# Kernel tuning notes

Measured on AMD Instinct MI355X. Metric: run time of the kernel, lower is better.

## Reference

```python
import jax, jax.numpy as jnp
import numpy as np
import math

B, S, HID, NH = 4, 2048, 1024, 16
HD = HID // NH  # head dim = 64


def setup_inputs() -> dict:
    key = jax.random.key(0)
    ks = jax.random.split(key, 8)
    sc = 0.02
    return {
        "x": jax.random.normal(ks[0], (B, S, HID), dtype=jnp.float32),
        "att_mask": jnp.zeros((B, 1, 1, S), dtype=jnp.float32),
        "Wq": jax.random.normal(ks[1], (HID, HID), dtype=jnp.float32) * sc,
        "bq": jax.random.normal(ks[2], (HID,), dtype=jnp.float32) * sc,
        "Wk": jax.random.normal(ks[3], (HID, HID), dtype=jnp.float32) * sc,
        "bk": jax.random.normal(ks[4], (HID,), dtype=jnp.float32) * sc,
        "Wv": jax.random.normal(ks[5], (HID, HID), dtype=jnp.float32) * sc,
        "bv": jax.random.normal(ks[6], (HID,), dtype=jnp.float32) * sc,
    }


def reference(x, att_mask, Wq, bq, Wk, bk, Wv, bv):
    # quant_mode=False path: QuantLinear acts as a plain affine projection
    # (the running min/max stats only calibrate `scale`, which is unused in
    # the float path), and IntSoftmax reduces to a standard softmax.
    q = x @ Wq.T + bq  # [B,S,HID]
    k = x @ Wk.T + bk
    v = x @ Wv.T + bv
    # split heads: [B,S,HID] -> [B,NH,S,HD]
    q = q.reshape(B, S, NH, HD).transpose(0, 2, 1, 3)
    k = k.reshape(B, S, NH, HD).transpose(0, 2, 1, 3)
    v = v.reshape(B, S, NH, HD).transpose(0, 2, 1, 3)
    scores = jnp.einsum("bhqd,bhkd->bhqk", q, k) / math.sqrt(HD) + att_mask
    probs = jax.nn.softmax(scores, axis=-1)  # [B,NH,S,S]
    ctx = jnp.einsum("bhqk,bhkd->bhqd", probs, v)  # [B,NH,S,HD]
    return ctx.transpose(0, 2, 1, 3).reshape(B, S, HID)
```

## Files before the change

### kernel.cpp

```cpp
#include <hip/hip_runtime.h>
#include <hip/hip_bf16.h>
#include <cstdint>
#include <cstddef>

#define BB   4
#define SS   2048
#define HIDD 1024
#define NHH  16
#define HDD  64
#define MM   (BB*SS)
#define L2E  1.4426950408889634f
#define SH4  5.770780163555854f

typedef __bf16    bf16x8 __attribute__((ext_vector_type(8)));
typedef float     f32x4  __attribute__((ext_vector_type(4)));
typedef _Float16  half4  __attribute__((ext_vector_type(4)));
typedef _Float16  half2v __attribute__((ext_vector_type(2)));

__device__ __forceinline__ unsigned short f2b(float f) {
    unsigned u = __builtin_bit_cast(unsigned, f);
    return (unsigned short)((u + 0x7FFFu + ((u >> 16) & 1u)) >> 16);
}

__device__ __forceinline__ half2v pkrtz(float a, float b) {
    return __builtin_bit_cast(half2v, __builtin_amdgcn_cvt_pkrtz(a, b));
}

__device__ __forceinline__ void gl_lds16(const void* g, void* l) {
    __builtin_amdgcn_global_load_lds(
        (const __attribute__((address_space(1))) void*)g,
        (__attribute__((address_space(3))) void*)l, 16, 0, 0);
}

#define NX4 (MM * HIDD / 4)
#define NW4 (HIDD * HIDD / 4)
__global__ __launch_bounds__(256) void cvt_all(
    const float* __restrict__ x,  const float* __restrict__ wq,
    const float* __restrict__ wk, const float* __restrict__ wv,
    unsigned short* __restrict__ xb, unsigned short* __restrict__ wb)
{
    int i = blockIdx.x * 256 + threadIdx.x;
    const float* src; unsigned short* dst; int off;
    if (i < NX4) { src = x; dst = xb; off = i; }
    else {
        int j = i - NX4;
        int w = j >> 18;
        off = j & (NW4 - 1);
        src = (w == 0) ? wq : (w == 1) ? wk : wv;
        dst = wb + (size_t)w * HIDD * HIDD;
    }
    float4 v = reinterpret_cast<const float4*>(src)[off];
    ushort4 o;
    o.x = f2b(v.x); o.y = f2b(v.y); o.z = f2b(v.z); o.w = f2b(v.w);
    reinterpret_cast<ushort4*>(dst)[off] = o;
}

__global__ __launch_bounds__(256, 3) void qkv_gemm(
    const unsigned short* __restrict__ xb,
    const unsigned short* __restrict__ wb,
    const float* __restrict__ bq, const float* __restrict__ bk, const float* __restrict__ bv,
    unsigned short* __restrict__ Qb, unsigned short* __restrict__ Kb,
    _Float16* __restrict__ Vtb)
{
    __shared__ unsigned short lA[128 * 64];
    __shared__ unsigned short lB[128 * 64];

    const int tid  = threadIdx.x;
    const int wave = tid >> 6, lane = tid & 63;
    const int lh   = lane & 15, quad = lane >> 4;
    const int l7   = lh & 7;
    const int m0   = blockIdx.x * 128;
    const int opn  = blockIdx.y;
    const int op   = opn >> 3;
    const int n0   = (opn & 7) * 128;
    const unsigned short* W = wb + (size_t)op * HIDD * HIDD;
    const float* bias = (op == 0) ? bq : (op == 1) ? bk : bv;

    f32x4 acc[4][4];
#pragma unroll
    for (int i = 0; i < 4; i++)
#pragma unroll
        for (int j = 0; j < 4; j++) acc[i][j] = f32x4{0.f, 0.f, 0.f, 0.f};

    const int wm = wave & 1, wn = wave >> 1;
    const unsigned short* srcA = (op == 2) ? lA : lB;
    const unsigned short* srcB = (op == 2) ? lB : lA;
    const int offA = (op == 2) ? wm : wn;
    const int offB = (op == 2) ? wn : wm;

    const int srow = tid >> 3;
    const int sg   = tid & 7;

    for (int k0 = 0; k0 < HIDD; k0 += 64) {
#pragma unroll
        for (int rr = 0; rr < 4; rr++) {
            const int row = srow + rr * 32;
            const int gcol = k0 + ((sg ^ (row & 7)) << 3);
            gl_lds16(&xb[(size_t)(m0 + row) * HIDD + gcol], &lA[row * 64 + sg * 8]);
            gl_lds16(&W [(size_t)(n0 + row) * HIDD + gcol], &lB[row * 64 + sg * 8]);
        }
        __syncthreads();

#pragma unroll
        for (int kk = 0; kk < 2; kk++) {
            bf16x8 aF[4], bF[4];
#pragma unroll
            for (int i = 0; i < 4; i++) {
                const int row = offA * 64 + i * 16 + lh;
                aF[i] = *reinterpret_cast<const bf16x8*>(
                    &srcA[row * 64 + (((kk * 4 + quad) ^ l7) << 3)]);
            }
#pragma unroll
            for (int j = 0; j < 4; j++) {
                const int row = offB * 64 + j * 16 + lh;
                bF[j] = *reinterpret_cast<const bf16x8*>(
                    &srcB[row * 64 + (((kk * 4 + quad) ^ l7) << 3)]);
            }
#pragma unroll
            for (int i = 0; i < 4; i++)
#pragma unroll
                for (int j = 0; j < 4; j++)
                    acc[i][j] = __builtin_amdgcn_mfma_f32_16x16x32_bf16(aF[i], bF[j], acc[i][j], 0, 0, 0);
        }
        __syncthreads();
    }

    if (op == 2) {
#pragma unroll
        for (int j = 0; j < 4; j++) {
            const int n = n0 + offB * 64 + j * 16 + lh;
            const float bvv = bias[n];
            const int h = n >> 6, d = n & 63;
#pragma unroll
            for (int i = 0; i < 4; i++) {
                const int mrow = m0 + offA * 64 + i * 16 + quad * 4;
                const int b_ = mrow >> 11, s_ = mrow & 2047;
                half2v h01 = pkrtz(acc[i][j][0] + bvv, acc[i][j][1] + bvv);
                half2v h23 = pkrtz(acc[i][j][2] + bvv, acc[i][j][3] + bvv);
                half4 hv; hv[0] = h01[0]; hv[1] = h01[1]; hv[2] = h23[0]; hv[3] = h23[1];
                size_t a = ((size_t)(b_ * NHH + h) * HDD + d) * SS + s_;
                *reinterpret_cast<half4*>(&Vtb[a]) = hv;
            }
        }
    } else {
        const float qs = (op == 0) ? (0.125f * L2E) : 1.0f;
        unsigned short* dst = (op == 0) ? Qb : Kb;
#pragma unroll
        for (int i = 0; i < 4; i++) {
            const int nb = n0 + offA * 64 + i * 16 + quad * 4;
            const float4 bb = *reinterpret_cast<const float4*>(&bias[nb]);
            const int h = nb >> 6, d = nb & 63;
#pragma unroll
            for (int j = 0; j < 4; j++) {
                const int m = m0 + offB * 64 + j * 16 + lh;
                const int b_ = m >> 11, s_ = m & 2047;
                ushort4 o;
                o.x = f2b((acc[i][j][0] + bb.x) * qs);
                o.y = f2b((acc[i][j][1] + bb.y) * qs);
                o.z = f2b((acc[i][j][2] + bb.z) * qs);
                o.w = f2b((acc[i][j][3] + bb.w) * qs);
                *reinterpret_cast<ushort4*>(
                    &dst[((size_t)(b_ * NHH + h) * SS + s_) * HDD + d]) = o;
            }
        }
    }
}

__global__ __launch_bounds__(256, 4) void attn_kernel(
    const unsigned short* __restrict__ Qb,
    const unsigned short* __restrict__ Kb,
    const _Float16* __restrict__ Vtb,
    const float* __restrict__ mask,
    float* __restrict__ out)
{
    __shared__ unsigned short lK[2][64 * 64];
    __shared__ _Float16      lV[2][64 * 64];

    const int tid  = threadIdx.x;
    const int wave = tid >> 6, lane = tid & 63;
    const int lh   = lane & 15, quad = lane >> 4;
    const int l7   = lh & 7;
    const int bh = blockIdx.x, qt = blockIdx.y;
    const int b = bh >> 4, h = bh & 15;
    const unsigned short* Qh = Qb  + (size_t)bh * SS * HDD;
    const unsigned short* Kh = Kb  + (size_t)bh * SS * HDD;
    const _Float16*       Vh = Vtb + (size_t)bh * HDD * SS;
    const float* mk = mask + (size_t)b * SS;
    const int q0 = qt * 128;

    bf16x8 qF[2][2];
#pragma unroll
    for (int i = 0; i < 2; i++)
#pragma unroll
        for (int kk = 0; kk < 2; kk++)
            qF[i][kk] = *reinterpret_cast<const bf16x8*>(
                &Qh[(size_t)(q0 + wave * 32 + i * 16 + lh) * HDD + kk * 32 + quad * 8]);

    f32x4 oacc[2][4];
#pragma unroll
    for (int i = 0; i < 2; i++)
#pragma unroll
        for (int dj = 0; dj < 4; dj++) oacc[i][dj] = f32x4{0.f, 0.f, 0.f, 0.f};
    float ls[2] = {0.f, 0.f};

    const int srow = tid >> 3;
    const int sg   = tid & 7;

#define STAGE(KT, BUF) do {                                                     \
    const int kb_ = (KT) * 64;                                                  \
    _Pragma("unroll")                                                           \
    for (int rr = 0; rr < 2; rr++) {                                            \
        const int row = srow + rr * 32;                                         \
        const int sw = ((sg ^ (row & 7)) << 3);                                 \
        gl_lds16(&Kh[(size_t)(kb_ + row) * HDD + sw], &lK[BUF][row * 64 + sg * 8]); \
        gl_lds16(&Vh[(size_t)row * SS + kb_ + sw],    &lV[BUF][row * 64 + sg * 8]); \
    }                                                                           \
} while (0)

    STAGE(0, 0);
    __syncthreads();

    for (int kt = 0; kt < SS / 64; kt++) {
        if (kt < SS / 64 - 1) STAGE(kt + 1, (kt + 1) & 1);
        const int buf = kt & 1;
        const int kb = kt * 64;

        float4 mg[4];
#pragma unroll
        for (int c = 0; c < 4; c++)
            mg[c] = *reinterpret_cast<const float4*>(&mk[kb + c * 16 + quad * 4]);

        half4 pf[4][2];
#pragma unroll
        for (int c = 0; c < 4; c++) {
            const int krow = (c * 16 + lh) * 64;
            bf16x8 kf0 = *reinterpret_cast<const bf16x8*>(&lK[buf][krow + ((quad ^ l7) << 3)]);
            bf16x8 kf1 = *reinterpret_cast<const bf16x8*>(&lK[buf][krow + (((4 + quad) ^ l7) << 3)]);
            f32x4 mm;
            mm[0] = __builtin_fmaf(mg[c].x, L2E, -SH4);
            mm[1] = __builtin_fmaf(mg[c].y, L2E, -SH4);
            mm[2] = __builtin_fmaf(mg[c].z, L2E, -SH4);
            mm[3] = __builtin_fmaf(mg[c].w, L2E, -SH4);
#pragma unroll
            for (int i = 0; i < 2; i++) {
                f32x4 s = __builtin_amdgcn_mfma_f32_16x16x32_bf16(kf0, qF[i][0], mm, 0, 0, 0);
                s = __builtin_amdgcn_mfma_f32_16x16x32_bf16(kf1, qF[i][1], s, 0, 0, 0);
                float e0 = __builtin_amdgcn_exp2f(s[0]);
                float e1 = __builtin_amdgcn_exp2f(s[1]);
                float e2 = __builtin_amdgcn_exp2f(s[2]);
                float e3 = __builtin_amdgcn_exp2f(s[3]);
                ls[i] += (e0 + e1) + (e2 + e3);
                half2v p01 = pkrtz(e0, e1);
                half2v p23 = pkrtz(e2, e3);
                half4 p; p[0] = p01[0]; p[1] = p01[1]; p[2] = p23[0]; p[3] = p23[1];
                pf[c][i] = p;
            }
        }

#pragma unroll
        for (int c = 0; c < 4; c++) {
            const int vg = (c * 2 + (quad >> 1)) ^ l7;
            half4 vf[4];
#pragma unroll
            for (int dj = 0; dj < 4; dj++)
                vf[dj] = *reinterpret_cast<const half4*>(
                    &lV[buf][(dj * 16 + lh) * 64 + (vg << 3) + (quad & 1) * 4]);
#pragma unroll
            for (int i = 0; i < 2; i++)
#pragma unroll
                for (int dj = 0; dj < 4; dj++)
                    oacc[i][dj] = __builtin_amdgcn_mfma_f32_16x16x16f16(vf[dj], pf[c][i], oacc[i][dj], 0, 0, 0);
        }
        if (kt < SS / 64 - 1) __syncthreads();
    }

    float rls[2];
#pragma unroll
    for (int i = 0; i < 2; i++) {
        float l = ls[i];
        l += __shfl_xor(l, 16);
        l += __shfl_xor(l, 32);
        rls[i] = 1.0f / l;
    }
#pragma unroll
    for (int i = 0; i < 2; i++) {
        const int q = q0 + wave * 32 + i * 16 + lh;
#pragma unroll
        for (int dj = 0; dj < 4; dj++) {
            float4 o4;
            o4.x = oacc[i][dj][0] * rls[i];
            o4.y = oacc[i][dj][1] * rls[i];
            o4.z = oacc[i][dj][2] * rls[i];
            o4.w = oacc[i][dj][3] * rls[i];
            *reinterpret_cast<float4*>(
                &out[((size_t)b * SS + q) * HIDD + h * HDD + dj * 16 + quad * 4]) = o4;
        }
    }
}

extern "C" void kernel_launch(void* const* d_in, const int* in_sizes, int n_in,
                              void* d_out, int out_size, void* d_ws, size_t ws_size,
                              hipStream_t stream) {
    const float* x    = (const float*)d_in[0];
    const float* mask = (const float*)d_in[1];
    const float* Wq   = (const float*)d_in[2];
    const float* bq   = (const float*)d_in[3];
    const float* Wk   = (const float*)d_in[4];
    const float* bk   = (const float*)d_in[5];
    const float* Wv   = (const float*)d_in[6];
    const float* bv   = (const float*)d_in[7];
    float* out = (float*)d_out;
    (void)in_sizes; (void)n_in; (void)out_size; (void)ws_size;

    unsigned short* ws  = (unsigned short*)d_ws;
    unsigned short* xb  = ws;
    unsigned short* wb  = xb + (size_t)MM * HIDD;
    unsigned short* Qb  = wb + (size_t)3 * HIDD * HIDD;
    unsigned short* Kb  = Qb + (size_t)MM * HIDD;
    _Float16*       Vtb = (_Float16*)(Kb + (size_t)MM * HIDD);

    cvt_all<<<(NX4 + 3 * NW4) / 256, 256, 0, stream>>>(x, Wq, Wk, Wv, xb, wb);

    qkv_gemm<<<dim3(MM / 128, 24), 256, 0, stream>>>(xb, wb, bq, bk, bv, Qb, Kb, Vtb);

    attn_kernel<<<dim3(BB * NHH, SS / 128), 256, 0, stream>>>(Qb, Kb, Vtb, mask, out);
}
```

Baseline: 242.4 us.

## Use 16x16x32 f16 MFMA for PV with permuted key order and swizzle

Replaces the PV product's 16x16x16 f16 MFMAs with 16x16x32 f16 MFMAs, halving the instruction count per key tile. Keys are permuted so each lane's score outputs form a contiguous 8-wide P fragment. The K LDS swizzle is changed to match the new row order, and V is read as 8-element vectors. The goal is higher matrix-core throughput and fewer LDS reads, at the cost of more complex indexing and possible bank-conflict changes.

After: 247.1 us. No clear change (+2.0%).

```diff
diff --git a/kernel.cpp b/kernel.cpp
--- a/kernel.cpp
+++ b/kernel.cpp
@@ -15,6 +15,7 @@
 typedef __bf16    bf16x8 __attribute__((ext_vector_type(8)));
 typedef float     f32x4  __attribute__((ext_vector_type(4)));
 typedef _Float16  half4  __attribute__((ext_vector_type(4)));
+typedef _Float16  half8  __attribute__((ext_vector_type(8)));
 typedef _Float16  half2v __attribute__((ext_vector_type(2)));
 
 __device__ __forceinline__ unsigned short f2b(float f) {
@@ -211,9 +212,10 @@
     _Pragma("unroll")                                                           \
     for (int rr = 0; rr < 2; rr++) {                                            \
         const int row = srow + rr * 32;                                         \
-        const int sw = ((sg ^ (row & 7)) << 3);                                 \
-        gl_lds16(&Kh[(size_t)(kb_ + row) * HDD + sw], &lK[BUF][row * 64 + sg * 8]); \
-        gl_lds16(&Vh[(size_t)row * SS + kb_ + sw],    &lV[BUF][row * 64 + sg * 8]); \
+        const int swk = ((sg ^ ((row & 3) | ((row >> 1) & 4))) << 3);           \
+        const int swv = ((sg ^ (row & 7)) << 3);                                \
+        gl_lds16(&Kh[(size_t)(kb_ + row) * HDD + swk], &lK[BUF][row * 64 + sg * 8]); \
+        gl_lds16(&Vh[(size_t)row * SS + kb_ + swv],    &lV[BUF][row * 64 + sg * 8]); \
     }                                                                           \
 } while (0)
 
@@ -227,49 +229,61 @@
 
         float4 mg[4];
 #pragma unroll
-        for (int c = 0; c < 4; c++)
-            mg[c] = *reinterpret_cast<const float4*>(&mk[kb + c * 16 + quad * 4]);
-
-        half4 pf[4][2];
-#pragma unroll
-        for (int c = 0; c < 4; c++) {
-            const int krow = (c * 16 + lh) * 64;
-            bf16x8 kf0 = *reinterpret_cast<const bf16x8*>(&lK[buf][krow + ((quad ^ l7) << 3)]);
-            bf16x8 kf1 = *reinterpret_cast<const bf16x8*>(&lK[buf][krow + (((4 + quad) ^ l7) << 3)]);
-            f32x4 mm;
-            mm[0] = __builtin_fmaf(mg[c].x, L2E, -SH4);
-            mm[1] = __builtin_fmaf(mg[c].y, L2E, -SH4);
-            mm[2] = __builtin_fmaf(mg[c].z, L2E, -SH4);
-            mm[3] = __builtin_fmaf(mg[c].w, L2E, -SH4);
-#pragma unroll
-            for (int i = 0; i < 2; i++) {
-                f32x4 s = __builtin_amdgcn_mfma_f32_16x16x32_bf16(kf0, qF[i][0], mm, 0, 0, 0);
-                s = __builtin_amdgcn_mfma_f32_16x16x32_bf16(kf1, qF[i][1], s, 0, 0, 0);
-                float e0 = __builtin_amdgcn_exp2f(s[0]);
-                float e1 = __builtin_amdgcn_exp2f(s[1]);
-                float e2 = __builtin_amdgcn_exp2f(s[2]);
-                float e3 = __builtin_amdgcn_exp2f(s[3]);
-                ls[i] += (e0 + e1) + (e2 + e3);
-                half2v p01 = pkrtz(e0, e1);
-                half2v p23 = pkrtz(e2, e3);
-                half4 p; p[0] = p01[0]; p[1] = p01[1]; p[2] = p23[0]; p[3] = p23[1];
-                pf[c][i] = p;
-            }
-        }
-
-#pragma unroll
-        for (int c = 0; c < 4; c++) {
-            const int vg = (c * 2 + (quad >> 1)) ^ l7;
-            half4 vf[4];
+        for (int t = 0; t < 2; t++)
+#pragma unroll
+            for (int a = 0; a < 2; a++)
+                mg[t * 2 + a] = *reinterpret_cast<const float4*>(
+                    &mk[kb + t * 32 + quad * 8 + a * 4]);
+
+        half8 pf[2][2];
+#pragma unroll
+        for (int t = 0; t < 2; t++) {
+#pragma unroll
+            for (int a = 0; a < 2; a++) {
+                const int key = t * 32 + ((lh & 12) << 1) + (a << 2) + (lh & 3);
+                const int krow = key * 64;
+                bf16x8 kf0 = *reinterpret_cast<const bf16x8*>(
+                    &lK[buf][krow + ((quad ^ l7) << 3)]);
+                bf16x8 kf1 = *reinterpret_cast<const bf16x8*>(
+                    &lK[buf][krow + (((4 + quad) ^ l7) << 3)]);
+                const float4 m4 = mg[t * 2 + a];
+                f32x4 mm;
+                mm[0] = __builtin_fmaf(m4.x, L2E, -SH4);
+                mm[1] = __builtin_fmaf(m4.y, L2E, -SH4);
+                mm[2] = __builtin_fmaf(m4.z, L2E, -SH4);
+                mm[3] = __builtin_fmaf(m4.w, L2E, -SH4);
+#pragma unroll
+                for (int i = 0; i < 2; i++) {
+                    f32x4 s = __builtin_amdgcn_mfma_f32_16x16x32_bf16(kf0, qF[i][0], mm, 0, 0, 0);
+                    s = __builtin_amdgcn_mfma_f32_16x16x32_bf16(kf1, qF[i][1], s, 0, 0, 0);
+                    float e0 = __builtin_amdgcn_exp2f(s[0]);
+                    float e1 = __builtin_amdgcn_exp2f(s[1]);
+                    float e2 = __builtin_amdgcn_exp2f(s[2]);
+                    float e3 = __builtin_amdgcn_exp2f(s[3]);
+                    ls[i] += (e0 + e1) + (e2 + e3);
+                    half2v p01 = pkrtz(e0, e1);
+                    half2v p23 = pkrtz(e2, e3);
+                    pf[t][i][a * 4 + 0] = p01[0];
+                    pf[t][i][a * 4 + 1] = p01[1];
+                    pf[t][i][a * 4 + 2] = p23[0];
+                    pf[t][i][a * 4 + 3] = p23[1];
+                }
+            }
+        }
+
+#pragma unroll
+        for (int t = 0; t < 2; t++) {
+            half8 vf[4];
 #pragma unroll
             for (int dj = 0; dj < 4; dj++)
-                vf[dj] = *reinterpret_cast<const half4*>(
-                    &lV[buf][(dj * 16 + lh) * 64 + (vg << 3) + (quad & 1) * 4]);
+                vf[dj] = *reinterpret_cast<const half8*>(
+                    &lV[buf][(dj * 16 + lh) * 64 + (((t * 4 + quad) ^ l7) << 3)]);
 #pragma unroll
             for (int i = 0; i < 2; i++)
 #pragma unroll
                 for (int dj = 0; dj < 4; dj++)
-                    oacc[i][dj] = __builtin_amdgcn_mfma_f32_16x16x16f16(vf[dj], pf[c][i], oacc[i][dj], 0, 0, 0);
+                    oacc[i][dj] = __builtin_amdgcn_mfma_f32_16x16x32_f16(
+                        vf[dj], pf[t][i], oacc[i][dj], 0, 0, 0);
         }
         if (kt < SS / 64 - 1) __syncthreads();
     }
```

## Software-pipeline QK softmax with PV, load V directly to registers

Applied to the files above, without the earlier changes.

Restructures the attention inner loop so the QK^T MFMA and exp phase for the next key tile runs ahead of the PV MFMAs of the current tile, using ping-pong probability registers and s_setprio around the PV block. V fragments are loaded straight from global memory into registers, with keys permuted so the PV step can use 16x16x32 f16 MFMA, and the V LDS buffer is dropped. The mask is precomputed once into LDS, and K staging is moved two tiles ahead. Occupancy hint drops from 4 to 3 waves per SIMD, trading occupancy for higher register pressure and direct global V loads inside the loop.

Result: slower. 368.7 us (+52.1%).

```diff
diff --git a/kernel.cpp b/kernel.cpp
--- a/kernel.cpp
+++ b/kernel.cpp
@@ -15,7 +15,9 @@
 typedef __bf16    bf16x8 __attribute__((ext_vector_type(8)));
 typedef float     f32x4  __attribute__((ext_vector_type(4)));
 typedef _Float16  half4  __attribute__((ext_vector_type(4)));
+typedef _Float16  half8  __attribute__((ext_vector_type(8)));
 typedef _Float16  half2v __attribute__((ext_vector_type(2)));
+typedef unsigned  u32x4  __attribute__((ext_vector_type(4)));
 
 __device__ __forceinline__ unsigned short f2b(float f) {
     unsigned u = __builtin_bit_cast(unsigned, f);
@@ -24,6 +26,10 @@
 
 __device__ __forceinline__ half2v pkrtz(float a, float b) {
     return __builtin_bit_cast(half2v, __builtin_amdgcn_cvt_pkrtz(a, b));
+}
+
+__device__ __forceinline__ unsigned pkrtz_u(float a, float b) {
+    return __builtin_bit_cast(unsigned, __builtin_amdgcn_cvt_pkrtz(a, b));
 }
 
 __device__ __forceinline__ void gl_lds16(const void* g, void* l) {
@@ -166,7 +172,7 @@
     }
 }
 
-__global__ __launch_bounds__(256, 4) void attn_kernel(
+__global__ __launch_bounds__(256, 3) void attn_kernel(
     const unsigned short* __restrict__ Qb,
     const unsigned short* __restrict__ Kb,
     const _Float16* __restrict__ Vtb,
@@ -174,7 +180,7 @@
     float* __restrict__ out)
 {
     __shared__ unsigned short lK[2][64 * 64];
-    __shared__ _Float16      lV[2][64 * 64];
+    __shared__ float         lmm[SS];
 
     const int tid  = threadIdx.x;
     const int wave = tid >> 6, lane = tid & 63;
@@ -206,72 +212,96 @@
     const int srow = tid >> 3;
     const int sg   = tid & 7;
 
-#define STAGE(KT, BUF) do {                                                     \
-    const int kb_ = (KT) * 64;                                                  \
-    _Pragma("unroll")                                                           \
-    for (int rr = 0; rr < 2; rr++) {                                            \
-        const int row = srow + rr * 32;                                         \
-        const int sw = ((sg ^ (row & 7)) << 3);                                 \
-        gl_lds16(&Kh[(size_t)(kb_ + row) * HDD + sw], &lK[BUF][row * 64 + sg * 8]); \
-        gl_lds16(&Vh[(size_t)row * SS + kb_ + sw],    &lV[BUF][row * 64 + sg * 8]); \
-    }                                                                           \
+#define STAGE_K(KT, BUF) do {                                                  \
+    const int kb_ = (KT) * 64;                                                 \
+    _Pragma("unroll")                                                          \
+    for (int rr = 0; rr < 2; rr++) {                                           \
+        const int row = srow + rr * 32;                                        \
+        const int swk = ((sg ^ ((row & 3) | ((row >> 1) & 4))) << 3);          \
+        gl_lds16(&Kh[(size_t)(kb_ + row) * HDD + swk], &lK[BUF][row * 64 + sg * 8]); \
+    }                                                                          \
 } while (0)
 
-    STAGE(0, 0);
+#define PHASE_A(KT, PF) do {                                                   \
+    const int bufA = (KT) & 1;                                                 \
+    const int kbA  = (KT) * 64;                                                \
+    _Pragma("unroll")                                                          \
+    for (int t = 0; t < 2; t++) {                                              \
+        _Pragma("unroll")                                                      \
+        for (int a = 0; a < 2; a++) {                                          \
+            const int key = t * 32 + ((lh & 12) << 1) + (a << 2) + (lh & 3);   \
+            const int krow = key * 64;                                         \
+            bf16x8 kf0 = *reinterpret_cast<const bf16x8*>(                     \
+                &lK[bufA][krow + ((quad ^ l7) << 3)]);                         \
+            bf16x8 kf1 = *reinterpret_cast<const bf16x8*>(                     \
+                &lK[bufA][krow + (((4 + quad) ^ l7) << 3)]);                   \
+            const f32x4 mm = *reinterpret_cast<const f32x4*>(                  \
+                &lmm[kbA + t * 32 + quad * 8 + a * 4]);                        \
+            _Pragma("unroll")                                                  \
+            for (int i = 0; i < 2; i++) {                                      \
+                f32x4 s = __builtin_amdgcn_mfma_f32_16x16x32_bf16(kf0, qF[i][0], mm, 0, 0, 0); \
+                s = __builtin_amdgcn_mfma_f32_16x16x32_bf16(kf1, qF[i][1], s, 0, 0, 0);        \
+                float e0 = __builtin_amdgcn_exp2f(s[0]);                       \
+                float e1 = __builtin_amdgcn_exp2f(s[1]);                       \
+                float e2 = __builtin_amdgcn_exp2f(s[2]);                       \
+                float e3 = __builtin_amdgcn_exp2f(s[3]);                       \
+                ls[i] += (e0 + e1) + (e2 + e3);                                \
+                PF[t][i][a * 2 + 0] = pkrtz_u(e0, e1);                         \
+                PF[t][i][a * 2 + 1] = pkrtz_u(e2, e3);                         \
+            }                                                                  \
+        }                                                                      \
+    }                                                                          \
+} while (0)
+
+#define ITER(KT, PFC, PFN) do {                                                \
+    half8 vf[2][4];                                                            \
+    _Pragma("unroll")                                                          \
+    for (int t = 0; t < 2; t++)                                                \
+        _Pragma("unroll")                                                      \
+        for (int dj = 0; dj < 4; dj++)                                         \
+            vf[t][dj] = *reinterpret_cast<const half8*>(                       \
+                &Vh[(size_t)(dj * 16 + lh) * SS + (KT) * 64 + t * 32 + quad * 8]); \
+    if ((KT) + 2 < 32) STAGE_K((KT) + 2, (KT) & 1);                            \
+    if ((KT) + 1 < 32) PHASE_A((KT) + 1, PFN);                                 \
+    __builtin_amdgcn_s_setprio(1);                                             \
+    _Pragma("unroll")                                                          \
+    for (int t = 0; t < 2; t++) {                                              \
+        _Pragma("unroll")                                                      \
+        for (int i = 0; i < 2; i++) {                                          \
+            const u32x4 pu = {PFC[t][i][0], PFC[t][i][1], PFC[t][i][2], PFC[t][i][3]}; \
+            const half8 pF = __builtin_bit_cast(half8, pu);                    \
+            _Pragma("unroll")                                                  \
+            for (int dj = 0; dj < 4; dj++)                                     \
+                oacc[i][dj] = __builtin_amdgcn_mfma_f32_16x16x32_f16(          \
+                    vf[t][dj], pF, oacc[i][dj], 0, 0, 0);                      \
+        }                                                                      \
+    }                                                                          \
+    __builtin_amdgcn_s_setprio(0);                                             \
+    if ((KT) < 31) __syncthreads();                                            \
+} while (0)
+
+    STAGE_K(0, 0);
+    STAGE_K(1, 1);
+#pragma unroll
+    for (int j = 0; j < 2; j++) {
+        const int idx = tid * 8 + j * 4;
+        float4 m = *reinterpret_cast<const float4*>(&mk[idx]);
+        float4 r;
+        r.x = __builtin_fmaf(m.x, L2E, -SH4);
+        r.y = __builtin_fmaf(m.y, L2E, -SH4);
+        r.z = __builtin_fmaf(m.z, L2E, -SH4);
+        r.w = __builtin_fmaf(m.w, L2E, -SH4);
+        *reinterpret_cast<float4*>(&lmm[idx]) = r;
+    }
     __syncthreads();
 
-    for (int kt = 0; kt < SS / 64; kt++) {
-        if (kt < SS / 64 - 1) STAGE(kt + 1, (kt + 1) & 1);
-        const int buf = kt & 1;
-        const int kb = kt * 64;
-
-        float4 mg[4];
-#pragma unroll
-        for (int c = 0; c < 4; c++)
-            mg[c] = *reinterpret_cast<const float4*>(&mk[kb + c * 16 + quad * 4]);
-
-        half4 pf[4][2];
-#pragma unroll
-        for (int c = 0; c < 4; c++) {
-            const int krow = (c * 16 + lh) * 64;
-            bf16x8 kf0 = *reinterpret_cast<const bf16x8*>(&lK[buf][krow + ((quad ^ l7) << 3)]);
-            bf16x8 kf1 = *reinterpret_cast<const bf16x8*>(&lK[buf][krow + (((4 + quad) ^ l7) << 3)]);
-            f32x4 mm;
-            mm[0] = __builtin_fmaf(mg[c].x, L2E, -SH4);
-            mm[1] = __builtin_fmaf(mg[c].y, L2E, -SH4);
-            mm[2] = __builtin_fmaf(mg[c].z, L2E, -SH4);
-            mm[3] = __builtin_fmaf(mg[c].w, L2E, -SH4);
-#pragma unroll
-            for (int i = 0; i < 2; i++) {
-                f32x4 s = __builtin_amdgcn_mfma_f32_16x16x32_bf16(kf0, qF[i][0], mm, 0, 0, 0);
-                s = __builtin_amdgcn_mfma_f32_16x16x32_bf16(kf1, qF[i][1], s, 0, 0, 0);
-                float e0 = __builtin_amdgcn_exp2f(s[0]);
-                float e1 = __builtin_amdgcn_exp2f(s[1]);
-                float e2 = __builtin_amdgcn_exp2f(s[2]);
-                float e3 = __builtin_amdgcn_exp2f(s[3]);
-                ls[i] += (e0 + e1) + (e2 + e3);
-                half2v p01 = pkrtz(e0, e1);
-                half2v p23 = pkrtz(e2, e3);
-                half4 p; p[0] = p01[0]; p[1] = p01[1]; p[2] = p23[0]; p[3] = p23[1];
-                pf[c][i] = p;
-            }
-        }
-
-#pragma unroll
-        for (int c = 0; c < 4; c++) {
-            const int vg = (c * 2 + (quad >> 1)) ^ l7;
-            half4 vf[4];
-#pragma unroll
-            for (int dj = 0; dj < 4; dj++)
-                vf[dj] = *reinterpret_cast<const half4*>(
-                    &lV[buf][(dj * 16 + lh) * 64 + (vg << 3) + (quad & 1) * 4]);
-#pragma unroll
-            for (int i = 0; i < 2; i++)
-#pragma unroll
-                for (int dj = 0; dj < 4; dj++)
-                    oacc[i][dj] = __builtin_amdgcn_mfma_f32_16x16x16f16(vf[dj], pf[c][i], oacc[i][dj], 0, 0, 0);
-        }
-        if (kt < SS / 64 - 1) __syncthreads();
+    unsigned pfA[2][2][4], pfB[2][2][4];
+    PHASE_A(0, pfA);
+    __syncthreads();
+
+    for (int kt = 0; kt < 32; kt += 2) {
+        ITER(kt,     pfA, pfB);
+        ITER(kt + 1, pfB, pfA);
     }
 
     float rls[2];
@@ -296,6 +326,9 @@
                 &out[((size_t)b * SS + q) * HIDD + h * HDD + dj * 16 + quad * 4]) = o4;
         }
     }
+#undef ITER
+#undef PHASE_A
+#undef STAGE_K
 }
 
 extern "C" void kernel_launch(void* const* d_in, const int* in_sizes, int n_in,
```
